# Performance work log

Measured on AMD Instinct MI355X. Metric: run time of the kernel, lower is better.

Reference implementation:

```python
import jax, jax.numpy as jnp
import numpy as np

DT = 3600.0  # integration step [s], module-level constant in the source
N_STEPS = 1_048_576


def _build_abc(rc):
    """Build continuous-time LTI matrices of the 4R3C thermal network.

    rc[:4] -> resistances (Rg, Ri, Re, Rw), rc[4:] -> capacitances (Cai, Cwe, Cwi).
    Raw rc values are in (0,1); rescale to physically plausible ranges so that
    explicit Euler with dt=3600 s is stable (|dt * eig(A)| << 1).
    """
    Rg, Ri, Re, Rw = (rc[:4] * 10.0 + 1.0)          # K/W-ish
    Cai, Cwe, Cwi = (rc[4:] * 1e6 + 1e5)            # J/K-ish
    A = jnp.array([
        [-(1.0 / Rg + 1.0 / Ri) / Cai, 0.0, 1.0 / (Ri * Cai)],
        [0.0, -(1.0 / Re + 1.0 / Rw) / Cwe, 1.0 / (Rw * Cwe)],
        [1.0 / (Ri * Cwi), 1.0 / (Rw * Cwi), -(1.0 / Rw + 1.0 / Ri) / Cwi],
    ], dtype=rc.dtype)
    B = jnp.array([
        [1.0 / (Rg * Cai), 1.0 / Cai, 1.0 / Cai, 0.0, 0.0],
        [1.0 / (Re * Cwe), 0.0, 0.0, 1.0 / Cwe, 0.0],
        [0.0, 0.0, 0.0, 0.0, 1.0 / Cwi],
    ], dtype=rc.dtype)
    Cm = jnp.array([[1.0, 0.0, 0.0]], dtype=rc.dtype)  # y = Tai
    return A, B, Cm


def setup_inputs() -> dict:
    key = jax.random.key(0)
    k1, k2, k3 = jax.random.split(key, 3)
    x_init = jax.random.normal(k1, (3,), dtype=jnp.float32)
    u = jax.random.normal(k2, (N_STEPS, 5), dtype=jnp.float32)
    rc = jax.random.uniform(k3, (7,), dtype=jnp.float32)
    return {"x_init": x_init, "u": u, "rc": rc}


def reference(x_init, u, rc):
    A, B, Cm = _build_abc(rc)

    def step(x, ut):
        # model(xi, ui): rhs = A x + B u, y = C x  (y from pre-update state)
        dx = A @ x + B @ ut
        y = Cm @ x
        x_new = x + dx * DT  # explicit Euler
        return x_new, (x_new, y)

    _, (xsol, ysol) = jax.lax.scan(step, x_init, u)
    return xsol, ysol  # [T,3], [T,1]
```

## Files before the change

### kernel.cpp

```cpp
#include <hip/hip_runtime.h>

#define DTSTEP  3600.0
#define T_STEPS 1048576
#define LCH     8
#define TPB     512
#define NBLK    256
#define MAGIC   0x51CAFE17u


__device__ inline void matsq3(double* C){
  double R[9];
#pragma unroll
  for (int r=0;r<3;r++){
#pragma unroll
    for (int c=0;c<3;c++){
      R[r*3+c] = C[r*3+0]*C[0+c] + C[r*3+1]*C[3+c] + C[r*3+2]*C[6+c];
    }
  }
#pragma unroll
  for (int k=0;k<9;k++) C[k]=R[k];
}

__device__ void setup_from_rc(const float* __restrict__ rc,
                              float* __restrict__ sMN, float* __restrict__ sPW){
  const float Rg = rc[0]*10.f+1.f, Ri = rc[1]*10.f+1.f, Re = rc[2]*10.f+1.f, Rw = rc[3]*10.f+1.f;
  const float Cai = rc[4]*1e6f+1e5f, Cwe = rc[5]*1e6f+1e5f, Cwi = rc[6]*1e6f+1e5f;
  double Md[9];
  Md[0] = 1.0 + DTSTEP*(-(1.0/Rg + 1.0/Ri)/Cai);
  Md[1] = 0.0;
  Md[2] = DTSTEP*(1.0/((double)Ri*(double)Cai));
  Md[3] = 0.0;
  Md[4] = 1.0 + DTSTEP*(-(1.0/Re + 1.0/Rw)/Cwe);
  Md[5] = DTSTEP*(1.0/((double)Rw*(double)Cwe));
  Md[6] = DTSTEP*(1.0/((double)Ri*(double)Cwi));
  Md[7] = DTSTEP*(1.0/((double)Rw*(double)Cwi));
  Md[8] = 1.0 + DTSTEP*(-(1.0/Rw + 1.0/Ri)/Cwi);
  sMN[0]=(float)Md[0]; sMN[1]=(float)Md[2]; sMN[2]=(float)Md[4]; sMN[3]=(float)Md[5];
  sMN[4]=(float)Md[6]; sMN[5]=(float)Md[7]; sMN[6]=(float)Md[8];
  sMN[7] =(float)(DTSTEP*(1.0/((double)Rg*(double)Cai)));
  sMN[8] =(float)(DTSTEP*(1.0/(double)Cai));
  sMN[9] =(float)(DTSTEP*(1.0/(double)Cai));
  sMN[10]=(float)(DTSTEP*(1.0/((double)Re*(double)Cwe)));
  sMN[11]=(float)(DTSTEP*(1.0/(double)Cwe));
  sMN[12]=(float)(DTSTEP*(1.0/(double)Cwi));
  double C[9];
#pragma unroll
  for (int k=0;k<9;k++) C[k]=Md[k];
  for (int k=1;k<=19;k++){
    matsq3(C);
    if (k>=3){
#pragma unroll
      for (int j=0;j<9;j++) sPW[(k-3)*9+j] = (float)C[j];
    }
  }
}

struct MN { float M0,M2,M4,M5,M6,M7,M8, N0,N1,N2,N5,N8,N14; };

__device__ inline MN mn_from_lds(const float* __restrict__ sMN){
  MN p;
  p.M0=sMN[0]; p.M2=sMN[1]; p.M4=sMN[2]; p.M5=sMN[3];
  p.M6=sMN[4]; p.M7=sMN[5]; p.M8=sMN[6];
  p.N0=sMN[7]; p.N1=sMN[8]; p.N2=sMN[9];
  p.N5=sMN[10]; p.N8=sMN[11]; p.N14=sMN[12];
  return p;
}

__device__ inline void chunk_v(const float* uu, const MN& mn, float& v0, float& v1, float& v2){
  v0=0.f; v1=0.f; v2=0.f;
#pragma unroll
  for (int j=0;j<LCH;j++){
    const float u0=uu[j*5+0],u1=uu[j*5+1],u2=uu[j*5+2],u3=uu[j*5+3],u4v=uu[j*5+4];
    const float c0 = fmaf(mn.N0,u0, fmaf(mn.N1,u1, mn.N2*u2));
    const float c1 = fmaf(mn.N5,u0, mn.N8*u3);
    const float c2 = mn.N14*u4v;
    const float n0 = fmaf(mn.M0,v0, fmaf(mn.M2,v2, c0));
    const float n1 = fmaf(mn.M4,v1, fmaf(mn.M5,v2, c1));
    const float n2 = fmaf(mn.M6,v0, fmaf(mn.M7,v1, fmaf(mn.M8,v2, c2)));
    v0=n0; v1=n1; v2=n2;
  }
}

__device__ inline void apply_pow(const float* __restrict__ sPW, int base, unsigned e,
                                 float& x0, float& x1, float& x2){
#pragma unroll
  for (int r=0;r<9;r++){
    if (e & (1u<<r)){
      const float* Q = &sPW[(base+r)*9];
      const float y0 = fmaf(Q[0],x0, fmaf(Q[1],x1, Q[2]*x2));
      const float y1 = fmaf(Q[3],x0, fmaf(Q[4],x1, Q[5]*x2));
      const float y2 = fmaf(Q[6],x0, fmaf(Q[7],x1, Q[8]*x2));
      x0=y0; x1=y1; x2=y2;
    }
  }
}

__global__ __launch_bounds__(TPB, 2) void k_fused(const float* __restrict__ u,
                                                  const float* __restrict__ rc,
                                                  const float* __restrict__ x_init,
                                                  float* __restrict__ wsAgg,
                                                  unsigned int* __restrict__ wsFlag,
                                                  float* __restrict__ out){
  __shared__ float sMN[13];
  __shared__ float sPW[17*9];
  __shared__ float buf[2][TPB*3];
  __shared__ float partial[8][3];
  __shared__ float sS[3];
  const int tid = threadIdx.x;
  const int blk = blockIdx.x;
  const int i   = blk*TPB + tid;
  float uu[LCH*5];
  const float4* u4 = reinterpret_cast<const float4*>(u) + (size_t)i*(LCH*5/4);
#pragma unroll
  for (int k=0;k<LCH*5/4;k++){
    const float4 q = u4[k];
    uu[k*4+0]=q.x; uu[k*4+1]=q.y; uu[k*4+2]=q.z; uu[k*4+3]=q.w;
  }
  if (tid==0) setup_from_rc(rc, sMN, sPW);
  __syncthreads();
  const MN mn = mn_from_lds(sMN);
  float t0,t1,t2;
  chunk_v(uu, mn, t0,t1,t2);
  buf[0][tid*3+0]=t0; buf[0][tid*3+1]=t1; buf[0][tid*3+2]=t2;
  __syncthreads();
  int cur=0;
#pragma unroll
  for (int r=0;r<9;r++){
    const int d = 1<<r;
    const float Q0=sPW[r*9+0],Q1=sPW[r*9+1],Q2=sPW[r*9+2],
                Q3=sPW[r*9+3],Q4=sPW[r*9+4],Q5=sPW[r*9+5],
                Q6=sPW[r*9+6],Q7=sPW[r*9+7],Q8=sPW[r*9+8];
    float p0=0.f,p1=0.f,p2=0.f;
    if (tid >= d){
      const int s=(tid-d)*3;
      p0=buf[cur][s+0]; p1=buf[cur][s+1]; p2=buf[cur][s+2];
    }
    t0 = fmaf(Q0,p0, fmaf(Q1,p1, fmaf(Q2,p2, t0)));
    t1 = fmaf(Q3,p0, fmaf(Q4,p1, fmaf(Q5,p2, t1)));
    t2 = fmaf(Q6,p0, fmaf(Q7,p1, fmaf(Q8,p2, t2)));
    buf[cur^1][tid*3+0]=t0; buf[cur^1][tid*3+1]=t1; buf[cur^1][tid*3+2]=t2;
    __syncthreads();
    cur ^= 1;
  }
  if (tid==TPB-1){
    __hip_atomic_store(&wsAgg[blk*3+0], t0, __ATOMIC_RELAXED, __HIP_MEMORY_SCOPE_AGENT);
    __hip_atomic_store(&wsAgg[blk*3+1], t1, __ATOMIC_RELAXED, __HIP_MEMORY_SCOPE_AGENT);
    __hip_atomic_store(&wsAgg[blk*3+2], t2, __ATOMIC_RELAXED, __HIP_MEMORY_SCOPE_AGENT);
    __hip_atomic_store(&wsFlag[blk], MAGIC, __ATOMIC_RELEASE, __HIP_MEMORY_SCOPE_AGENT);
  }
  float c0=0.f, c1=0.f, c2=0.f;
  if (tid < blk){
    while (__hip_atomic_load(&wsFlag[tid], __ATOMIC_ACQUIRE, __HIP_MEMORY_SCOPE_AGENT) != MAGIC){}
    c0=__hip_atomic_load(&wsAgg[tid*3+0], __ATOMIC_RELAXED, __HIP_MEMORY_SCOPE_AGENT);
    c1=__hip_atomic_load(&wsAgg[tid*3+1], __ATOMIC_RELAXED, __HIP_MEMORY_SCOPE_AGENT);
    c2=__hip_atomic_load(&wsAgg[tid*3+2], __ATOMIC_RELAXED, __HIP_MEMORY_SCOPE_AGENT);
    apply_pow(sPW, 9, (unsigned)(blk-1-tid), c0,c1,c2);
  } else if (tid==TPB-1){
    c0=x_init[0]; c1=x_init[1]; c2=x_init[2];
    apply_pow(sPW, 9, (unsigned)blk, c0,c1,c2);
  }
#pragma unroll
  for (int off=32; off>0; off>>=1){
    c0 += __shfl_down(c0, off, 64);
    c1 += __shfl_down(c1, off, 64);
    c2 += __shfl_down(c2, off, 64);
  }
  if ((tid & 63)==0){
    partial[tid>>6][0]=c0; partial[tid>>6][1]=c1; partial[tid>>6][2]=c2;
  }
  __syncthreads();
  if (tid==0){
    float S0=0.f,S1=0.f,S2=0.f;
#pragma unroll
    for (int w=0;w<8;w++){ S0+=partial[w][0]; S1+=partial[w][1]; S2+=partial[w][2]; }
    sS[0]=S0; sS[1]=S1; sS[2]=S2;
  }
  __syncthreads();
  float x0=sS[0], x1=sS[1], x2=sS[2];
  apply_pow(sPW, 0, (unsigned)tid, x0,x1,x2);
  if (tid>0){
    const int s=(tid-1)*3;
    x0 += buf[cur][s+0]; x1 += buf[cur][s+1]; x2 += buf[cur][s+2];
  }
  float px[LCH*3], py[LCH];
#pragma unroll
  for (int j=0;j<LCH;j++){
    py[j]=x0;
    const float u0=uu[j*5+0],u1=uu[j*5+1],u2=uu[j*5+2],u3=uu[j*5+3],u4v=uu[j*5+4];
    const float c0v = fmaf(mn.N0,u0, fmaf(mn.N1,u1, mn.N2*u2));
    const float c1v = fmaf(mn.N5,u0, mn.N8*u3);
    const float c2v = mn.N14*u4v;
    const float n0 = fmaf(mn.M0,x0, fmaf(mn.M2,x2, c0v));
    const float n1 = fmaf(mn.M4,x1, fmaf(mn.M5,x2, c1v));
    const float n2 = fmaf(mn.M6,x0, fmaf(mn.M7,x1, fmaf(mn.M8,x2, c2v)));
    x0=n0; x1=n1; x2=n2;
    px[j*3+0]=x0; px[j*3+1]=x1; px[j*3+2]=x2;
  }
  float4* xo4 = reinterpret_cast<float4*>(out) + (size_t)i*6;
#pragma unroll
  for (int m=0;m<6;m++)
    xo4[m] = make_float4(px[4*m+0],px[4*m+1],px[4*m+2],px[4*m+3]);
  float4* yo4 = reinterpret_cast<float4*>(out) + (size_t)(3*T_STEPS/4) + (size_t)i*2;
  yo4[0] = make_float4(py[0],py[1],py[2],py[3]);
  yo4[1] = make_float4(py[4],py[5],py[6],py[7]);
}

extern "C" void kernel_launch(void* const* d_in, const int* in_sizes, int n_in,
                              void* d_out, int out_size, void* d_ws, size_t ws_size,
                              hipStream_t stream) {
  (void)out_size; (void)ws_size;
  const float* x_init = (const float*)d_in[0];
  const float* u      = (const float*)d_in[1];
  const float* rc     = (const float*)d_in[2];
  for (int k=0;k<n_in;k++){
    if (in_sizes[k]==3) x_init = (const float*)d_in[k];
    else if (in_sizes[k]==7) rc = (const float*)d_in[k];
    else if (in_sizes[k]==T_STEPS*5) u = (const float*)d_in[k];
  }
  float* wsAgg = (float*)d_ws;
  unsigned int* wsFlag = (unsigned int*)((float*)d_ws + 1024);
  float* out = (float*)d_out;

  k_fused<<<NBLK, TPB, 0, stream>>>(u, rc, x_init, wsAgg, wsFlag, out);
}
```

Baseline: 28.22 us.

## Replace LDS block scan with wave-shuffle scan plus cross-wave combine

Replaces the 9-round shared-memory Hillis-Steele scan, which needed a __syncthreads per round, with a 6-round intra-wave scan using __shfl_up. A second 3-round scan over the 8 wave aggregates runs in wave 0, so the block aggregate is published after only a couple of barriers. The cross-block spin-wait now polls relaxed with s_sleep and does a single acquire load afterwards, and the final prefix is rebuilt from the wave offset, then the lane power, then the shuffled predecessor. The goal is to cut barrier latency on the serial lookback critical path, in exchange for extra reconstruction work per thread and dropping the occupancy hint of 2 from launch_bounds.

```diff
diff --git a/kernel.cpp b/kernel.cpp
--- a/kernel.cpp
+++ b/kernel.cpp
@@ -81,12 +81,13 @@
   }
 }
 
-__device__ inline void apply_pow(const float* __restrict__ sPW, int base, unsigned e,
-                                 float& x0, float& x1, float& x2){
-#pragma unroll
-  for (int r=0;r<9;r++){
+template<int BASE, int NBITS>
+__device__ inline void apply_pw(const float* __restrict__ sPW, unsigned e,
+                                float& x0, float& x1, float& x2){
+#pragma unroll
+  for (int r=0;r<NBITS;r++){
     if (e & (1u<<r)){
-      const float* Q = &sPW[(base+r)*9];
+      const float* Q = &sPW[(BASE+r)*9];
       const float y0 = fmaf(Q[0],x0, fmaf(Q[1],x1, Q[2]*x2));
       const float y1 = fmaf(Q[3],x0, fmaf(Q[4],x1, Q[5]*x2));
       const float y2 = fmaf(Q[6],x0, fmaf(Q[7],x1, Q[8]*x2));
@@ -95,20 +96,22 @@
   }
 }
 
-__global__ __launch_bounds__(TPB, 2) void k_fused(const float* __restrict__ u,
-                                                  const float* __restrict__ rc,
-                                                  const float* __restrict__ x_init,
-                                                  float* __restrict__ wsAgg,
-                                                  unsigned int* __restrict__ wsFlag,
-                                                  float* __restrict__ out){
+__global__ __launch_bounds__(TPB) void k_fused(const float* __restrict__ u,
+                                               const float* __restrict__ rc,
+                                               const float* __restrict__ x_init,
+                                               float* __restrict__ wsAgg,
+                                               unsigned int* __restrict__ wsFlag,
+                                               float* __restrict__ out){
   __shared__ float sMN[13];
   __shared__ float sPW[17*9];
-  __shared__ float buf[2][TPB*3];
+  __shared__ float wagg[8][3];
+  __shared__ float woff[8][3];
   __shared__ float partial[8][3];
-  __shared__ float sS[3];
-  const int tid = threadIdx.x;
-  const int blk = blockIdx.x;
-  const int i   = blk*TPB + tid;
+  const int tid  = threadIdx.x;
+  const int blk  = blockIdx.x;
+  const int lane = tid & 63;
+  const int wid  = tid >> 6;
+  const int i    = blk*TPB + tid;
   float uu[LCH*5];
   const float4* u4 = reinterpret_cast<const float4*>(u) + (size_t)i*(LCH*5/4);
 #pragma unroll
@@ -119,80 +122,95 @@
   if (tid==0) setup_from_rc(rc, sMN, sPW);
   __syncthreads();
   const MN mn = mn_from_lds(sMN);
-  float t0,t1,t2;
-  chunk_v(uu, mn, t0,t1,t2);
-  buf[0][tid*3+0]=t0; buf[0][tid*3+1]=t1; buf[0][tid*3+2]=t2;
-  __syncthreads();
-  int cur=0;
-#pragma unroll
-  for (int r=0;r<9;r++){
+  float L0,L1,L2;
+  chunk_v(uu, mn, L0,L1,L2);
+#pragma unroll
+  for (int r=0;r<6;r++){
     const int d = 1<<r;
-    const float Q0=sPW[r*9+0],Q1=sPW[r*9+1],Q2=sPW[r*9+2],
-                Q3=sPW[r*9+3],Q4=sPW[r*9+4],Q5=sPW[r*9+5],
-                Q6=sPW[r*9+6],Q7=sPW[r*9+7],Q8=sPW[r*9+8];
-    float p0=0.f,p1=0.f,p2=0.f;
-    if (tid >= d){
-      const int s=(tid-d)*3;
-      p0=buf[cur][s+0]; p1=buf[cur][s+1]; p2=buf[cur][s+2];
-    }
-    t0 = fmaf(Q0,p0, fmaf(Q1,p1, fmaf(Q2,p2, t0)));
-    t1 = fmaf(Q3,p0, fmaf(Q4,p1, fmaf(Q5,p2, t1)));
-    t2 = fmaf(Q6,p0, fmaf(Q7,p1, fmaf(Q8,p2, t2)));
-    buf[cur^1][tid*3+0]=t0; buf[cur^1][tid*3+1]=t1; buf[cur^1][tid*3+2]=t2;
-    __syncthreads();
-    cur ^= 1;
-  }
-  if (tid==TPB-1){
-    __hip_atomic_store(&wsAgg[blk*3+0], t0, __ATOMIC_RELAXED, __HIP_MEMORY_SCOPE_AGENT);
-    __hip_atomic_store(&wsAgg[blk*3+1], t1, __ATOMIC_RELAXED, __HIP_MEMORY_SCOPE_AGENT);
-    __hip_atomic_store(&wsAgg[blk*3+2], t2, __ATOMIC_RELAXED, __HIP_MEMORY_SCOPE_AGENT);
-    __hip_atomic_store(&wsFlag[blk], MAGIC, __ATOMIC_RELEASE, __HIP_MEMORY_SCOPE_AGENT);
-  }
+    const float* Q = &sPW[r*9];
+    const float p0=__shfl_up(L0,(unsigned)d,64);
+    const float p1=__shfl_up(L1,(unsigned)d,64);
+    const float p2=__shfl_up(L2,(unsigned)d,64);
+    if (lane >= d){
+      const float y0 = fmaf(Q[0],p0, fmaf(Q[1],p1, fmaf(Q[2],p2, L0)));
+      const float y1 = fmaf(Q[3],p0, fmaf(Q[4],p1, fmaf(Q[5],p2, L1)));
+      const float y2 = fmaf(Q[6],p0, fmaf(Q[7],p1, fmaf(Q[8],p2, L2)));
+      L0=y0; L1=y1; L2=y2;
+    }
+  }
+  if (lane==63){ wagg[wid][0]=L0; wagg[wid][1]=L1; wagg[wid][2]=L2; }
+  __syncthreads();
+  if (wid==0){
+    float a0=0.f,a1=0.f,a2=0.f;
+    if (lane<8){ a0=wagg[lane][0]; a1=wagg[lane][1]; a2=wagg[lane][2]; }
+#pragma unroll
+    for (int r=0;r<3;r++){
+      const int d = 1<<r;
+      const float* Q = &sPW[(6+r)*9];
+      const float p0=__shfl_up(a0,(unsigned)d,64);
+      const float p1=__shfl_up(a1,(unsigned)d,64);
+      const float p2=__shfl_up(a2,(unsigned)d,64);
+      if (lane>=d && lane<8){
+        const float y0 = fmaf(Q[0],p0, fmaf(Q[1],p1, fmaf(Q[2],p2, a0)));
+        const float y1 = fmaf(Q[3],p0, fmaf(Q[4],p1, fmaf(Q[5],p2, a1)));
+        const float y2 = fmaf(Q[6],p0, fmaf(Q[7],p1, fmaf(Q[8],p2, a2)));
+        a0=y0; a1=y1; a2=y2;
+      }
+    }
+    if (lane==7){
+      __hip_atomic_store(&wsAgg[blk*3+0], a0, __ATOMIC_RELAXED, __HIP_MEMORY_SCOPE_AGENT);
+      __hip_atomic_store(&wsAgg[blk*3+1], a1, __ATOMIC_RELAXED, __HIP_MEMORY_SCOPE_AGENT);
+      __hip_atomic_store(&wsAgg[blk*3+2], a2, __ATOMIC_RELAXED, __HIP_MEMORY_SCOPE_AGENT);
+      __hip_atomic_store(&wsFlag[blk], MAGIC, __ATOMIC_RELEASE, __HIP_MEMORY_SCOPE_AGENT);
+    }
+    if (lane<8){ woff[lane][0]=a0; woff[lane][1]=a1; woff[lane][2]=a2; }
+  }
+  __syncthreads();
   float c0=0.f, c1=0.f, c2=0.f;
   if (tid < blk){
-    while (__hip_atomic_load(&wsFlag[tid], __ATOMIC_ACQUIRE, __HIP_MEMORY_SCOPE_AGENT) != MAGIC){}
+    while (__hip_atomic_load(&wsFlag[tid], __ATOMIC_RELAXED, __HIP_MEMORY_SCOPE_AGENT) != MAGIC)
+      __builtin_amdgcn_s_sleep(2);
+    (void)__hip_atomic_load(&wsFlag[tid], __ATOMIC_ACQUIRE, __HIP_MEMORY_SCOPE_AGENT);
     c0=__hip_atomic_load(&wsAgg[tid*3+0], __ATOMIC_RELAXED, __HIP_MEMORY_SCOPE_AGENT);
     c1=__hip_atomic_load(&wsAgg[tid*3+1], __ATOMIC_RELAXED, __HIP_MEMORY_SCOPE_AGENT);
     c2=__hip_atomic_load(&wsAgg[tid*3+2], __ATOMIC_RELAXED, __HIP_MEMORY_SCOPE_AGENT);
-    apply_pow(sPW, 9, (unsigned)(blk-1-tid), c0,c1,c2);
+    apply_pw<9,8>(sPW, (unsigned)(blk-1-tid), c0,c1,c2);
   } else if (tid==TPB-1){
     c0=x_init[0]; c1=x_init[1]; c2=x_init[2];
-    apply_pow(sPW, 9, (unsigned)blk, c0,c1,c2);
+    apply_pw<9,8>(sPW, (unsigned)blk, c0,c1,c2);
   }
 #pragma unroll
   for (int off=32; off>0; off>>=1){
-    c0 += __shfl_down(c0, off, 64);
-    c1 += __shfl_down(c1, off, 64);
-    c2 += __shfl_down(c2, off, 64);
-  }
-  if ((tid & 63)==0){
-    partial[tid>>6][0]=c0; partial[tid>>6][1]=c1; partial[tid>>6][2]=c2;
-  }
-  __syncthreads();
-  if (tid==0){
-    float S0=0.f,S1=0.f,S2=0.f;
-#pragma unroll
-    for (int w=0;w<8;w++){ S0+=partial[w][0]; S1+=partial[w][1]; S2+=partial[w][2]; }
-    sS[0]=S0; sS[1]=S1; sS[2]=S2;
-  }
-  __syncthreads();
-  float x0=sS[0], x1=sS[1], x2=sS[2];
-  apply_pow(sPW, 0, (unsigned)tid, x0,x1,x2);
-  if (tid>0){
-    const int s=(tid-1)*3;
-    x0 += buf[cur][s+0]; x1 += buf[cur][s+1]; x2 += buf[cur][s+2];
+    c0 += __shfl_down(c0, (unsigned)off, 64);
+    c1 += __shfl_down(c1, (unsigned)off, 64);
+    c2 += __shfl_down(c2, (unsigned)off, 64);
+  }
+  if (lane==0){ partial[wid][0]=c0; partial[wid][1]=c1; partial[wid][2]=c2; }
+  __syncthreads();
+  float S0=0.f,S1=0.f,S2=0.f;
+#pragma unroll
+  for (int w=0;w<8;w++){ S0+=partial[w][0]; S1+=partial[w][1]; S2+=partial[w][2]; }
+  float x0=S0, x1=S1, x2=S2;
+  apply_pw<6,3>(sPW, (unsigned)wid, x0,x1,x2);
+  if (wid>0){ x0+=woff[wid-1][0]; x1+=woff[wid-1][1]; x2+=woff[wid-1][2]; }
+  apply_pw<0,6>(sPW, (unsigned)lane, x0,x1,x2);
+  {
+    const float q0=__shfl_up(L0,1u,64);
+    const float q1=__shfl_up(L1,1u,64);
+    const float q2=__shfl_up(L2,1u,64);
+    if (lane>0){ x0+=q0; x1+=q1; x2+=q2; }
   }
   float px[LCH*3], py[LCH];
 #pragma unroll
   for (int j=0;j<LCH;j++){
     py[j]=x0;
     const float u0=uu[j*5+0],u1=uu[j*5+1],u2=uu[j*5+2],u3=uu[j*5+3],u4v=uu[j*5+4];
-    const float c0v = fmaf(mn.N0,u0, fmaf(mn.N1,u1, mn.N2*u2));
-    const float c1v = fmaf(mn.N5,u0, mn.N8*u3);
-    const float c2v = mn.N14*u4v;
-    const float n0 = fmaf(mn.M0,x0, fmaf(mn.M2,x2, c0v));
-    const float n1 = fmaf(mn.M4,x1, fmaf(mn.M5,x2, c1v));
-    const float n2 = fmaf(mn.M6,x0, fmaf(mn.M7,x1, fmaf(mn.M8,x2, c2v)));
+    const float d0 = fmaf(mn.N0,u0, fmaf(mn.N1,u1, mn.N2*u2));
+    const float d1 = fmaf(mn.N5,u0, mn.N8*u3);
+    const float d2 = mn.N14*u4v;
+    const float n0 = fmaf(mn.M0,x0, fmaf(mn.M2,x2, d0));
+    const float n1 = fmaf(mn.M4,x1, fmaf(mn.M5,x2, d1));
+    const float n2 = fmaf(mn.M6,x0, fmaf(mn.M7,x1, fmaf(mn.M8,x2, d2)));
     x0=n0; x1=n1; x2=n2;
     px[j*3+0]=x0; px[j*3+1]=x1; px[j*3+2]=x2;
   }
```

Measured after the change: 29.00 us. 2.8% more time.
